# Kernel optimization log

Hardware: AMD Instinct MI355X
Metric: run time of the kernel (lower is better)

The kernel has to match this reference:

```python
import jax, jax.numpy as jnp
import numpy as np

B, IN, H = 4096, 512, 1024
ALPHA, RHO = 0.001, 0.05

def setup_inputs() -> dict:
    key = jax.random.key(0)
    ks = jax.random.split(key, 9)
    inp = jax.random.normal(ks[0], (B, IN), dtype=jnp.float32)
    time = jax.random.uniform(ks[1], (B, 1), dtype=jnp.float32) * 100.0
    hx = jax.random.normal(ks[2], (B, H), dtype=jnp.float32)
    cx = jax.random.normal(ks[3], (B, H), dtype=jnp.float32)
    # params (match torch init scales loosely)
    Wxh_w = jax.random.normal(ks[4], (4 * H, IN), dtype=jnp.float32) / np.sqrt(IN)
    Wxh_b = jnp.zeros((4 * H,), dtype=jnp.float32)
    Whh_w = jax.random.normal(ks[5], (4 * H, H), dtype=jnp.float32) / np.sqrt(H)
    tau = jax.random.normal(ks[6], (H,), dtype=jnp.float32) * 0.5 + 5.0
    s = jax.random.uniform(ks[7], (H,), dtype=jnp.float32) * tau
    alpha = jnp.array([ALPHA], dtype=jnp.float32)
    rho = jnp.array([RHO], dtype=jnp.float32)
    return {"input": inp, "time": time, "hx": hx, "cx": cx,
            "Wxh_w": Wxh_w, "Wxh_b": Wxh_b, "Whh_w": Whh_w,
            "tau": tau, "s": s, "alpha": alpha, "rho": rho}

def _time_gate(time, s, tau, alpha, rho):
    # phi: [B, H] (time [B,1] broadcast against s/tau [H])
    phi = jnp.fmod(time - s, tau) / tau
    k = jnp.where(phi < rho / 2.0, 2.0 * phi / rho,
        jnp.where(phi < rho, 2.0 - 2.0 * phi / rho, alpha * phi))
    # computed under torch.no_grad() in the original
    return jax.lax.stop_gradient(k)

def reference(input, time, hx, cx, Wxh_w, Wxh_b, Whh_w, tau, s, alpha, rho):
    gates = input @ Wxh_w.T + Wxh_b + hx @ Whh_w.T  # [B, 4H]
    i, f, g, o = jnp.split(gates, 4, axis=1)
    k = _time_gate(time, s, tau, alpha, rho)
    ft = jax.nn.sigmoid(f + 1.0 - k)
    it = jax.nn.sigmoid(i) * k
    gt = jnp.tanh(g) * k
    ot = jax.nn.sigmoid(o) * k
    cy = ft * cx + it * gt
    hy = ot * jnp.tanh(cy)
    return (hy, cy)
```

## Files before the change

kernel.cpp:

```cpp
#include <hip/hip_runtime.h>

#define AS1 __attribute__((address_space(1)))
#define AS3 __attribute__((address_space(3)))

typedef _Float16 half_t;
typedef __attribute__((ext_vector_type(8))) _Float16 f16x8;
typedef __attribute__((ext_vector_type(4))) float f32x4;

static constexpr int Bsz = 4096;
static constexpr int INs = 512;
static constexpr int Hs  = 1024;
static constexpr int BM  = 128;
static constexpr int BH  = 32;
static constexpr int BK  = 64;

static constexpr size_t XN  = (size_t)Bsz * INs;
static constexpr size_t HXN = (size_t)Bsz * Hs;
static constexpr size_t WXN = (size_t)4 * Hs * INs;
static constexpr size_t WHN = (size_t)4 * Hs * Hs;
static constexpr size_t OFF_X  = 0;
static constexpr size_t OFF_HX = XN;
static constexpr size_t OFF_WX = XN + HXN;
static constexpr size_t OFF_WH = XN + HXN + WXN;
static constexpr size_t TOT    = XN + HXN + WXN + WHN;
static constexpr size_t KN     = (size_t)Bsz * Hs;

__device__ __forceinline__ float sigm(float x) {
  return 1.0f / (1.0f + __expf(-x));
}
__device__ __forceinline__ float tanh_fast(float x) {
  const float e = __expf(2.0f * x);
  return 1.0f - 2.0f / (e + 1.0f);
}

__global__ __launch_bounds__(256)
void cvt_kernel(const float* __restrict__ x, const float* __restrict__ hx,
                const float* __restrict__ wx, const float* __restrict__ wh,
                const float* __restrict__ timep, const float* __restrict__ sp,
                const float* __restrict__ taup, const float* __restrict__ alphap,
                const float* __restrict__ rhop,
                half_t* __restrict__ ws, float* __restrict__ kout) {
  const size_t cid = (size_t)blockIdx.x * 256 + threadIdx.x;
  if (cid < TOT / 8) {
    const size_t e = cid * 8;
    const float* src; size_t off;
    if (e < OFF_HX)      { src = x;  off = e - OFF_X; }
    else if (e < OFF_WX) { src = hx; off = e - OFF_HX; }
    else if (e < OFF_WH) { src = wx; off = e - OFF_WX; }
    else                 { src = wh; off = e - OFF_WH; }
    const f32x4 a = *(const f32x4*)(src + off);
    const f32x4 b = *(const f32x4*)(src + off + 4);
    f16x8 o;
    o[0]=(half_t)a[0]; o[1]=(half_t)a[1]; o[2]=(half_t)a[2]; o[3]=(half_t)a[3];
    o[4]=(half_t)b[0]; o[5]=(half_t)b[1]; o[6]=(half_t)b[2]; o[7]=(half_t)b[3];
    *(f16x8*)(ws + e) = o;
  } else {
    const size_t e2 = (cid - TOT / 8) * 8;
    const int b = (int)(e2 >> 10);
    const int h = (int)(e2 & 1023);
    const float tv = timep[b];
    const float alphav = alphap[0];
    const float rhov   = rhop[0];
    const float rh     = 0.5f * rhov;
    const f32x4 s0 = *(const f32x4*)(sp + h),   s1 = *(const f32x4*)(sp + h + 4);
    const f32x4 t0 = *(const f32x4*)(taup + h), t1 = *(const f32x4*)(taup + h + 4);
    f32x4 k0, k1;
    #pragma unroll
    for (int j = 0; j < 8; ++j) {
      const float sv   = j < 4 ? s0[j] : s1[j - 4];
      const float tauv = j < 4 ? t0[j] : t1[j - 4];
      const float phi = fmodf(tv - sv, tauv) / tauv;
      float kv;
      if (phi < rh)        kv = (2.0f * phi) / rhov;
      else if (phi < rhov) kv = 2.0f - (2.0f * phi) / rhov;
      else                 kv = alphav * phi;
      if (j < 4) k0[j] = kv; else k1[j - 4] = kv;
    }
    *(f32x4*)(kout + e2) = k0;
    *(f32x4*)(kout + e2 + 4) = k1;
  }
}

template <int MODE>
__global__ __launch_bounds__(256, 3)
void plstm_gemm(const void* __restrict__ xin_,
                const float* __restrict__ timep,
                const void* __restrict__ hxp_,
                const float* __restrict__ cxp,
                const void* __restrict__ wxh_,
                const float* __restrict__ biasp,
                const void* __restrict__ whh_,
                const float* __restrict__ taup,
                const float* __restrict__ sp,
                const float* __restrict__ alphap,
                const float* __restrict__ rhop,
                const float* __restrict__ kp,
                float* __restrict__ outp)
{
  __shared__ half_t As[BM * BK];
  __shared__ half_t Bs[BM * BK];

  const int tid  = threadIdx.x;
  const int w    = tid >> 6;
  const int lane = tid & 63;
  const int l15  = lane & 15;
  const int grp  = lane >> 4;
  const int wr   = w >> 1;
  const int wc   = w & 1;

  const int m0 = blockIdx.x * BM;
  const int h0 = blockIdx.y * BH;

  f32x4 acc[4][4] = {};

  const int ldr = tid >> 3;
  const int ldc = tid & 7;

  for (int phase = 0; phase < 2; ++phase) {
    const void* Ap = (phase == 0) ? xin_ : hxp_;
    const void* Wp = (phase == 0) ? wxh_ : whh_;
    const int Ka = (phase == 0) ? INs : Hs;

    for (int k0 = 0; k0 < Ka; k0 += BK) {
      #pragma unroll
      for (int i = 0; i < 4; ++i) {
        const int e    = i * 32 + ldr;
        const int gc8  = ldc ^ (e & 7);
        const int wrow = ((e >> 4) & 3) * Hs + h0 + ((e >> 6) << 4) + (e & 15);
        if (MODE >= 1) {
          const half_t* ga = (const half_t*)Ap + (size_t)(m0 + e) * Ka + (k0 + gc8 * 8);
          __builtin_amdgcn_global_load_lds((AS1 void*)ga,
                                           (AS3 void*)(As + (e * 8 + ldc) * 8), 16, 0, 0);
          const half_t* gw = (const half_t*)Wp + (size_t)wrow * Ka + (k0 + gc8 * 8);
          __builtin_amdgcn_global_load_lds((AS1 void*)gw,
                                           (AS3 void*)(Bs + (e * 8 + ldc) * 8), 16, 0, 0);
        } else {
          const float* ga = (const float*)Ap + (size_t)(m0 + e) * Ka + (k0 + gc8 * 8);
          const f32x4 a0 = *(const f32x4*)ga, a1 = *(const f32x4*)(ga + 4);
          f16x8 pa;
          pa[0]=(half_t)a0[0]; pa[1]=(half_t)a0[1]; pa[2]=(half_t)a0[2]; pa[3]=(half_t)a0[3];
          pa[4]=(half_t)a1[0]; pa[5]=(half_t)a1[1]; pa[6]=(half_t)a1[2]; pa[7]=(half_t)a1[3];
          *(f16x8*)(As + (e * 8 + ldc) * 8) = pa;
          const float* gw = (const float*)Wp + (size_t)wrow * Ka + (k0 + gc8 * 8);
          const f32x4 b0 = *(const f32x4*)gw, b1 = *(const f32x4*)(gw + 4);
          f16x8 pb;
          pb[0]=(half_t)b0[0]; pb[1]=(half_t)b0[1]; pb[2]=(half_t)b0[2]; pb[3]=(half_t)b0[3];
          pb[4]=(half_t)b1[0]; pb[5]=(half_t)b1[1]; pb[6]=(half_t)b1[2]; pb[7]=(half_t)b1[3];
          *(f16x8*)(Bs + (e * 8 + ldc) * 8) = pb;
        }
      }
      __syncthreads();

      #pragma unroll
      for (int kk = 0; kk < 2; ++kk) {
        const int c8x = (kk * 4 + grp);
        f16x8 af[4], bfr[4];
        #pragma unroll
        for (int mt = 0; mt < 4; ++mt) {
          const int e = wr * 64 + mt * 16 + l15;
          af[mt] = *(const f16x8*)(As + (e * 8 + (c8x ^ (l15 & 7))) * 8);
        }
        #pragma unroll
        for (int nt = 0; nt < 4; ++nt) {
          const int e = wc * 64 + nt * 16 + l15;
          bfr[nt] = *(const f16x8*)(Bs + (e * 8 + (c8x ^ (l15 & 7))) * 8);
        }
        #pragma unroll
        for (int mt = 0; mt < 4; ++mt)
          #pragma unroll
          for (int nt = 0; nt < 4; ++nt)
            acc[mt][nt] = __builtin_amdgcn_mfma_f32_16x16x32_f16(
                af[mt], bfr[nt], acc[mt][nt], 0, 0, 0);
      }
      __syncthreads();
    }
  }

  const int h = h0 + wc * 16 + l15;
  const float bi  = biasp[h];
  const float bfv = biasp[Hs + h];
  const float bg  = biasp[2 * Hs + h];
  const float bo  = biasp[3 * Hs + h];

  float sv = 0.f, tauv = 1.f, alphav = 0.f, rhov = 1.f, rh = 0.f;
  if (MODE < 2) {
    sv = sp[h]; tauv = taup[h];
    alphav = alphap[0]; rhov = rhop[0]; rh = 0.5f * rhov;
  }

  #pragma unroll
  for (int mt = 0; mt < 4; ++mt) {
    #pragma unroll
    for (int r = 0; r < 4; ++r) {
      const int brow = m0 + wr * 64 + mt * 16 + grp * 4 + r;
      float kv;
      if (MODE == 2) {
        kv = kp[(size_t)brow * Hs + h];
      } else {
        const float tv = timep[brow];
        const float phi = fmodf(tv - sv, tauv) / tauv;
        if (phi < rh)        kv = (2.0f * phi) / rhov;
        else if (phi < rhov) kv = 2.0f - (2.0f * phi) / rhov;
        else                 kv = alphav * phi;
      }
      const float iv = acc[mt][0][r] + bi;
      const float fv = acc[mt][1][r] + bfv;
      const float gv = acc[mt][2][r] + bg;
      const float ov = acc[mt][3][r] + bo;

      const float cxv = cxp[(size_t)brow * Hs + h];
      const float ft = sigm(fv + 1.0f - kv);
      const float it = sigm(iv) * kv;
      const float gt = tanh_fast(gv) * kv;
      const float ot = sigm(ov) * kv;
      const float cy = ft * cxv + it * gt;
      const float hy = ot * tanh_fast(cy);

      outp[(size_t)brow * Hs + h] = hy;
      outp[(size_t)Bsz * Hs + (size_t)brow * Hs + h] = cy;
    }
  }
}

extern "C" void kernel_launch(void* const* d_in, const int* in_sizes, int n_in,
                              void* d_out, int out_size, void* d_ws, size_t ws_size,
                              hipStream_t stream) {
  (void)in_sizes; (void)n_in; (void)out_size;
  const float* xin   = (const float*)d_in[0];
  const float* timep = (const float*)d_in[1];
  const float* hxp   = (const float*)d_in[2];
  const float* cxp   = (const float*)d_in[3];
  const float* wxh   = (const float*)d_in[4];
  const float* biasp = (const float*)d_in[5];
  const float* whh   = (const float*)d_in[6];
  const float* taup  = (const float*)d_in[7];
  const float* sp    = (const float*)d_in[8];
  const float* alphap= (const float*)d_in[9];
  const float* rhop  = (const float*)d_in[10];
  float* outp = (float*)d_out;

  dim3 grid(Bsz / BM, Hs / BH);
  const bool wsF16 = ws_size >= TOT * sizeof(half_t);
  const bool wsK   = ws_size >= TOT * sizeof(half_t) + KN * sizeof(float);

  if (wsK) {
    half_t* ws = (half_t*)d_ws;
    float* kout = (float*)(ws + TOT);
    const int nchunk = (int)(TOT / 8 + KN / 8);
    cvt_kernel<<<nchunk / 256, 256, 0, stream>>>(xin, hxp, wxh, whh,
                                                 timep, sp, taup, alphap, rhop,
                                                 ws, kout);
    plstm_gemm<2><<<grid, 256, 0, stream>>>(
        ws + OFF_X, timep, ws + OFF_HX, cxp, ws + OFF_WX, biasp, ws + OFF_WH,
        taup, sp, alphap, rhop, kout, outp);
  } else if (wsF16) {
    half_t* ws = (half_t*)d_ws;
    cvt_kernel<<<(int)(TOT / 8 / 256), 256, 0, stream>>>(xin, hxp, wxh, whh,
                                                 timep, sp, taup, alphap, rhop,
                                                 ws, nullptr);
    plstm_gemm<1><<<grid, 256, 0, stream>>>(
        ws + OFF_X, timep, ws + OFF_HX, cxp, ws + OFF_WX, biasp, ws + OFF_WH,
        taup, sp, alphap, rhop, nullptr, outp);
  } else {
    plstm_gemm<0><<<grid, 256, 0, stream>>>(
        xin, timep, hxp, cxp, wxh, biasp, whh,
        taup, sp, alphap, rhop, nullptr, outp);
  }
}
```

Before: 206.0 us.

## Double-buffer LDS tiles in the fp16 GEMM path with flattened K loop

The fp16 workspace GEMM now keeps two LDS buffers for A and B and issues the asynchronous global-to-LDS loads for the next K tile before computing on the current one. The two phases (input and hidden) are merged into one flattened K loop, so there is one barrier per tile instead of two. This aims to hide global load latency behind the MFMA work. In exchange LDS use doubles and the occupancy hint drops from 3 to 2 blocks per CU. The intermediate fp16-only mode is removed and the fp32 fallback is split out into its own kernel.

Measured after the change: 206.5 us. No clear change (+0.2%).

```diff
diff --git a/kernel.cpp b/kernel.cpp
--- a/kernel.cpp
+++ b/kernel.cpp
@@ -13,6 +13,7 @@
 static constexpr int BM  = 128;
 static constexpr int BH  = 32;
 static constexpr int BK  = 64;
+static constexpr int NIT = INs / BK + Hs / BK;
 
 static constexpr size_t XN  = (size_t)Bsz * INs;
 static constexpr size_t HXN = (size_t)Bsz * Hs;
@@ -81,24 +82,18 @@
   }
 }
 
-template <int MODE>
-__global__ __launch_bounds__(256, 3)
-void plstm_gemm(const void* __restrict__ xin_,
-                const float* __restrict__ timep,
-                const void* __restrict__ hxp_,
-                const float* __restrict__ cxp,
-                const void* __restrict__ wxh_,
-                const float* __restrict__ biasp,
-                const void* __restrict__ whh_,
-                const float* __restrict__ taup,
-                const float* __restrict__ sp,
-                const float* __restrict__ alphap,
-                const float* __restrict__ rhop,
-                const float* __restrict__ kp,
-                float* __restrict__ outp)
+__global__ __launch_bounds__(256, 2)
+void plstm_gemm_db(const half_t* __restrict__ xin,
+                   const half_t* __restrict__ hxp,
+                   const float* __restrict__ cxp,
+                   const half_t* __restrict__ wxh,
+                   const float* __restrict__ biasp,
+                   const half_t* __restrict__ whh,
+                   const float* __restrict__ kp,
+                   float* __restrict__ outp)
 {
-  __shared__ half_t As[BM * BK];
-  __shared__ half_t Bs[BM * BK];
+  __shared__ half_t As[2][BM * BK];
+  __shared__ half_t Bs[2][BM * BK];
 
   const int tid  = threadIdx.x;
   const int w    = tid >> 6;
@@ -116,64 +111,55 @@
   const int ldr = tid >> 3;
   const int ldc = tid & 7;
 
-  for (int phase = 0; phase < 2; ++phase) {
-    const void* Ap = (phase == 0) ? xin_ : hxp_;
-    const void* Wp = (phase == 0) ? wxh_ : whh_;
-    const int Ka = (phase == 0) ? INs : Hs;
-
-    for (int k0 = 0; k0 < Ka; k0 += BK) {
-      #pragma unroll
-      for (int i = 0; i < 4; ++i) {
-        const int e    = i * 32 + ldr;
-        const int gc8  = ldc ^ (e & 7);
-        const int wrow = ((e >> 4) & 3) * Hs + h0 + ((e >> 6) << 4) + (e & 15);
-        if (MODE >= 1) {
-          const half_t* ga = (const half_t*)Ap + (size_t)(m0 + e) * Ka + (k0 + gc8 * 8);
-          __builtin_amdgcn_global_load_lds((AS1 void*)ga,
-                                           (AS3 void*)(As + (e * 8 + ldc) * 8), 16, 0, 0);
-          const half_t* gw = (const half_t*)Wp + (size_t)wrow * Ka + (k0 + gc8 * 8);
-          __builtin_amdgcn_global_load_lds((AS1 void*)gw,
-                                           (AS3 void*)(Bs + (e * 8 + ldc) * 8), 16, 0, 0);
-        } else {
-          const float* ga = (const float*)Ap + (size_t)(m0 + e) * Ka + (k0 + gc8 * 8);
-          const f32x4 a0 = *(const f32x4*)ga, a1 = *(const f32x4*)(ga + 4);
-          f16x8 pa;
-          pa[0]=(half_t)a0[0]; pa[1]=(half_t)a0[1]; pa[2]=(half_t)a0[2]; pa[3]=(half_t)a0[3];
-          pa[4]=(half_t)a1[0]; pa[5]=(half_t)a1[1]; pa[6]=(half_t)a1[2]; pa[7]=(half_t)a1[3];
-          *(f16x8*)(As + (e * 8 + ldc) * 8) = pa;
-          const float* gw = (const float*)Wp + (size_t)wrow * Ka + (k0 + gc8 * 8);
-          const f32x4 b0 = *(const f32x4*)gw, b1 = *(const f32x4*)(gw + 4);
-          f16x8 pb;
-          pb[0]=(half_t)b0[0]; pb[1]=(half_t)b0[1]; pb[2]=(half_t)b0[2]; pb[3]=(half_t)b0[3];
-          pb[4]=(half_t)b1[0]; pb[5]=(half_t)b1[1]; pb[6]=(half_t)b1[2]; pb[7]=(half_t)b1[3];
-          *(f16x8*)(Bs + (e * 8 + ldc) * 8) = pb;
-        }
+  auto stage = [&](int it, int buf) {
+    const bool p1 = it >= INs / BK;
+    const half_t* Ap = p1 ? hxp : xin;
+    const half_t* Wp = p1 ? whh : wxh;
+    const int Ka = p1 ? Hs : INs;
+    const int k0 = (p1 ? (it - INs / BK) : it) * BK;
+    #pragma unroll
+    for (int i = 0; i < 4; ++i) {
+      const int e    = i * 32 + ldr;
+      const int gc8  = ldc ^ (e & 7);
+      const int wrow = ((e >> 4) & 3) * Hs + h0 + ((e >> 6) << 4) + (e & 15);
+      const half_t* ga = Ap + (size_t)(m0 + e) * Ka + (k0 + gc8 * 8);
+      __builtin_amdgcn_global_load_lds((AS1 void*)ga,
+                                       (AS3 void*)(&As[buf][(e * 8 + ldc) * 8]), 16, 0, 0);
+      const half_t* gw = Wp + (size_t)wrow * Ka + (k0 + gc8 * 8);
+      __builtin_amdgcn_global_load_lds((AS1 void*)gw,
+                                       (AS3 void*)(&Bs[buf][(e * 8 + ldc) * 8]), 16, 0, 0);
+    }
+  };
+
+  stage(0, 0);
+  __syncthreads();
+
+  for (int it = 0; it < NIT; ++it) {
+    if (it + 1 < NIT) stage(it + 1, (it + 1) & 1);
+    const half_t* as = As[it & 1];
+    const half_t* bs = Bs[it & 1];
+    #pragma unroll
+    for (int kk = 0; kk < 2; ++kk) {
+      const int c8x = kk * 4 + grp;
+      f16x8 af[4], bfr[4];
+      #pragma unroll
+      for (int mt = 0; mt < 4; ++mt) {
+        const int e = wr * 64 + mt * 16 + l15;
+        af[mt] = *(const f16x8*)(as + (e * 8 + (c8x ^ (l15 & 7))) * 8);
       }
-      __syncthreads();
-
-      #pragma unroll
-      for (int kk = 0; kk < 2; ++kk) {
-        const int c8x = (kk * 4 + grp);
-        f16x8 af[4], bfr[4];
+      #pragma unroll
+      for (int nt = 0; nt < 4; ++nt) {
+        const int e = wc * 64 + nt * 16 + l15;
+        bfr[nt] = *(const f16x8*)(bs + (e * 8 + (c8x ^ (l15 & 7))) * 8);
+      }
+      #pragma unroll
+      for (int mt = 0; mt < 4; ++mt)
         #pragma unroll
-        for (int mt = 0; mt < 4; ++mt) {
-          const int e = wr * 64 + mt * 16 + l15;
-          af[mt] = *(const f16x8*)(As + (e * 8 + (c8x ^ (l15 & 7))) * 8);
-        }
-        #pragma unroll
-        for (int nt = 0; nt < 4; ++nt) {
-          const int e = wc * 64 + nt * 16 + l15;
-          bfr[nt] = *(const f16x8*)(Bs + (e * 8 + (c8x ^ (l15 & 7))) * 8);
-        }
-        #pragma unroll
-        for (int mt = 0; mt < 4; ++mt)
-          #pragma unroll
-          for (int nt = 0; nt < 4; ++nt)
-            acc[mt][nt] = __builtin_amdgcn_mfma_f32_16x16x32_f16(
-                af[mt], bfr[nt], acc[mt][nt], 0, 0, 0);
-      }
-      __syncthreads();
-    }
+        for (int nt = 0; nt < 4; ++nt)
+          acc[mt][nt] = __builtin_amdgcn_mfma_f32_16x16x32_f16(
+              af[mt], bfr[nt], acc[mt][nt], 0, 0, 0);
+    }
+    __syncthreads();
   }
 
   const int h = h0 + wc * 16 + l15;
@@ -182,27 +168,12 @@
   const float bg  = biasp[2 * Hs + h];
   const float bo  = biasp[3 * Hs + h];
 
-  float sv = 0.f, tauv = 1.f, alphav = 0.f, rhov = 1.f, rh = 0.f;
-  if (MODE < 2) {
-    sv = sp[h]; tauv = taup[h];
-    alphav = alphap[0]; rhov = rhop[0]; rh = 0.5f * rhov;
-  }
-
   #pragma unroll
   for (int mt = 0; mt < 4; ++mt) {
     #pragma unroll
     for (int r = 0; r < 4; ++r) {
       const int brow = m0 + wr * 64 + mt * 16 + grp * 4 + r;
-      float kv;
-      if (MODE == 2) {
-        kv = kp[(size_t)brow * Hs + h];
-      } else {
-        const float tv = timep[brow];
-        const float phi = fmodf(tv - sv, tauv) / tauv;
-        if (phi < rh)        kv = (2.0f * phi) / rhov;
-        else if (phi < rhov) kv = 2.0f - (2.0f * phi) / rhov;
-        else                 kv = alphav * phi;
-      }
+      const float kv = kp[(size_t)brow * Hs + h];
       const float iv = acc[mt][0][r] + bi;
       const float fv = acc[mt][1][r] + bfv;
       const float gv = acc[mt][2][r] + bg;
@@ -210,12 +181,123 @@
 
       const float cxv = cxp[(size_t)brow * Hs + h];
       const float ft = sigm(fv + 1.0f - kv);
-      const float it = sigm(iv) * kv;
+      const float it2 = sigm(iv) * kv;
       const float gt = tanh_fast(gv) * kv;
       const float ot = sigm(ov) * kv;
-      const float cy = ft * cxv + it * gt;
+      const float cy = ft * cxv + it2 * gt;
       const float hy = ot * tanh_fast(cy);
 
+      outp[(size_t)brow * Hs + h] = hy;
+      outp[(size_t)Bsz * Hs + (size_t)brow * Hs + h] = cy;
+    }
+  }
+}
+
+__global__ __launch_bounds__(256, 3)
+void plstm_gemm_f32(const float* __restrict__ xin, const float* __restrict__ timep,
+                    const float* __restrict__ hxp, const float* __restrict__ cxp,
+                    const float* __restrict__ wxh, const float* __restrict__ biasp,
+                    const float* __restrict__ whh, const float* __restrict__ taup,
+                    const float* __restrict__ sp, const float* __restrict__ alphap,
+                    const float* __restrict__ rhop, float* __restrict__ outp)
+{
+  __shared__ half_t As[BM * BK];
+  __shared__ half_t Bs[BM * BK];
+
+  const int tid  = threadIdx.x;
+  const int w    = tid >> 6;
+  const int lane = tid & 63;
+  const int l15  = lane & 15;
+  const int grp  = lane >> 4;
+  const int wr   = w >> 1;
+  const int wc   = w & 1;
+
+  const int m0 = blockIdx.x * BM;
+  const int h0 = blockIdx.y * BH;
+
+  f32x4 acc[4][4] = {};
+  const int ldr = tid >> 3;
+  const int ldc = tid & 7;
+
+  for (int it = 0; it < NIT; ++it) {
+    const bool p1 = it >= INs / BK;
+    const float* Ap = p1 ? hxp : xin;
+    const float* Wp = p1 ? whh : wxh;
+    const int Ka = p1 ? Hs : INs;
+    const int k0 = (p1 ? (it - INs / BK) : it) * BK;
+    #pragma unroll
+    for (int i = 0; i < 4; ++i) {
+      const int e    = i * 32 + ldr;
+      const int gc8  = ldc ^ (e & 7);
+      const int wrow = ((e >> 4) & 3) * Hs + h0 + ((e >> 6) << 4) + (e & 15);
+      const float* ga = Ap + (size_t)(m0 + e) * Ka + (k0 + gc8 * 8);
+      const f32x4 a0 = *(const f32x4*)ga, a1 = *(const f32x4*)(ga + 4);
+      f16x8 pa;
+      pa[0]=(half_t)a0[0]; pa[1]=(half_t)a0[1]; pa[2]=(half_t)a0[2]; pa[3]=(half_t)a0[3];
+      pa[4]=(half_t)a1[0]; pa[5]=(half_t)a1[1]; pa[6]=(half_t)a1[2]; pa[7]=(half_t)a1[3];
+      *(f16x8*)(As + (e * 8 + ldc) * 8) = pa;
+      const float* gw = Wp + (size_t)wrow * Ka + (k0 + gc8 * 8);
+      const f32x4 b0 = *(const f32x4*)gw, b1 = *(const f32x4*)(gw + 4);
+      f16x8 pb;
+      pb[0]=(half_t)b0[0]; pb[1]=(half_t)b0[1]; pb[2]=(half_t)b0[2]; pb[3]=(half_t)b0[3];
+      pb[4]=(half_t)b1[0]; pb[5]=(half_t)b1[1]; pb[6]=(half_t)b1[2]; pb[7]=(half_t)b1[3];
+      *(f16x8*)(Bs + (e * 8 + ldc) * 8) = pb;
+    }
+    __syncthreads();
+    #pragma unroll
+    for (int kk = 0; kk < 2; ++kk) {
+      const int c8x = kk * 4 + grp;
+      f16x8 af[4], bfr[4];
+      #pragma unroll
+      for (int mt = 0; mt < 4; ++mt) {
+        const int e = wr * 64 + mt * 16 + l15;
+        af[mt] = *(const f16x8*)(As + (e * 8 + (c8x ^ (l15 & 7))) * 8);
+      }
+      #pragma unroll
+      for (int nt = 0; nt < 4; ++nt) {
+        const int e = wc * 64 + nt * 16 + l15;
+        bfr[nt] = *(const f16x8*)(Bs + (e * 8 + (c8x ^ (l15 & 7))) * 8);
+      }
+      #pragma unroll
+      for (int mt = 0; mt < 4; ++mt)
+        #pragma unroll
+        for (int nt = 0; nt < 4; ++nt)
+          acc[mt][nt] = __builtin_amdgcn_mfma_f32_16x16x32_f16(
+              af[mt], bfr[nt], acc[mt][nt], 0, 0, 0);
+    }
+    __syncthreads();
+  }
+
+  const int h = h0 + wc * 16 + l15;
+  const float bi  = biasp[h];
+  const float bfv = biasp[Hs + h];
+  const float bg  = biasp[2 * Hs + h];
+  const float bo  = biasp[3 * Hs + h];
+  const float sv = sp[h], tauv = taup[h];
+  const float alphav = alphap[0], rhov = rhop[0], rh = 0.5f * rhov;
+
+  #pragma unroll
+  for (int mt = 0; mt < 4; ++mt) {
+    #pragma unroll
+    for (int r = 0; r < 4; ++r) {
+      const int brow = m0 + wr * 64 + mt * 16 + grp * 4 + r;
+      const float tv = timep[brow];
+      const float phi = fmodf(tv - sv, tauv) / tauv;
+      float kv;
+      if (phi < rh)        kv = (2.0f * phi) / rhov;
+      else if (phi < rhov) kv = 2.0f - (2.0f * phi) / rhov;
+      else                 kv = alphav * phi;
+      const float iv = acc[mt][0][r] + bi;
+      const float fv = acc[mt][1][r] + bfv;
+      const float gv = acc[mt][2][r] + bg;
+      const float ov = acc[mt][3][r] + bo;
+      const float cxv = cxp[(size_t)brow * Hs + h];
+      const float ft = sigm(fv + 1.0f - kv);
+      const float it2 = sigm(iv) * kv;
+      const float gt = tanh_fast(gv) * kv;
+      const float ot = sigm(ov) * kv;
+      const float cy = ft * cxv + it2 * gt;
+      const float hy = ot * tanh_fast(cy);
       outp[(size_t)brow * Hs + h] = hy;
       outp[(size_t)Bsz * Hs + (size_t)brow * Hs + h] = cy;
     }
@@ -240,8 +322,7 @@
   float* outp = (float*)d_out;
 
   dim3 grid(Bsz / BM, Hs / BH);
-  const bool wsF16 = ws_size >= TOT * sizeof(half_t);
-  const bool wsK   = ws_size >= TOT * sizeof(half_t) + KN * sizeof(float);
+  const bool wsK = ws_size >= TOT * sizeof(half_t) + KN * sizeof(float);
 
   if (wsK) {
     half_t* ws = (half_t*)d_ws;
@@ -250,20 +331,12 @@
     cvt_kernel<<<nchunk / 256, 256, 0, stream>>>(xin, hxp, wxh, whh,
                                                  timep, sp, taup, alphap, rhop,
                                                  ws, kout);
-    plstm_gemm<2><<<grid, 256, 0, stream>>>(
-        ws + OFF_X, timep, ws + OFF_HX, cxp, ws + OFF_WX, biasp, ws + OFF_WH,
-        taup, sp, alphap, rhop, kout, outp);
-  } else if (wsF16) {
-    half_t* ws = (half_t*)d_ws;
-    cvt_kernel<<<(int)(TOT / 8 / 256), 256, 0, stream>>>(xin, hxp, wxh, whh,
-                                                 timep, sp, taup, alphap, rhop,
-                                                 ws, nullptr);
-    plstm_gemm<1><<<grid, 256, 0, stream>>>(
-        ws + OFF_X, timep, ws + OFF_HX, cxp, ws + OFF_WX, biasp, ws + OFF_WH,
-        taup, sp, alphap, rhop, nullptr, outp);
+    plstm_gemm_db<<<grid, 256, 0, stream>>>(
+        ws + OFF_X, ws + OFF_HX, cxp, ws + OFF_WX, biasp, ws + OFF_WH,
+        kout, outp);
   } else {
-    plstm_gemm<0><<<grid, 256, 0, stream>>>(
+    plstm_gemm_f32<<<grid, 256, 0, stream>>>(
         xin, timep, hxp, cxp, wxh, biasp, whh,
-        taup, sp, alphap, rhop, nullptr, outp);
-  }
-}
+        taup, sp, alphap, rhop, outp);
+  }
+}
```

## Fuse fp32-to-fp16 conversion into GEMM loads and drop pre-conversion kernel

Applied to the files above, without the earlier changes.

Removes the separate conversion kernel that wrote fp16 copies of inputs and weights plus a precomputed time-gate tensor to workspace. The single fused kernel now loads fp32 directly, converts to fp16 in registers before storing to LDS, and computes the time gate inline. It also flattens the two-phase K loop into one loop and raises the occupancy hint to 4 blocks per SM. This avoids an extra pass over the weights and activations, but the GEMM now reads fp32 (twice the bytes) for every tile, repeatedly across blocks, and loses the async global-to-LDS loads.

Measured after the change: 215.5 us. 4.6% more time.

```diff
diff --git a/kernel.cpp b/kernel.cpp
--- a/kernel.cpp
+++ b/kernel.cpp
@@ -1,7 +1,4 @@
 #include <hip/hip_runtime.h>
-
-#define AS1 __attribute__((address_space(1)))
-#define AS3 __attribute__((address_space(3)))
 
 typedef _Float16 half_t;
 typedef __attribute__((ext_vector_type(8))) _Float16 f16x8;
@@ -13,17 +10,7 @@
 static constexpr int BM  = 128;
 static constexpr int BH  = 32;
 static constexpr int BK  = 64;
-
-static constexpr size_t XN  = (size_t)Bsz * INs;
-static constexpr size_t HXN = (size_t)Bsz * Hs;
-static constexpr size_t WXN = (size_t)4 * Hs * INs;
-static constexpr size_t WHN = (size_t)4 * Hs * Hs;
-static constexpr size_t OFF_X  = 0;
-static constexpr size_t OFF_HX = XN;
-static constexpr size_t OFF_WX = XN + HXN;
-static constexpr size_t OFF_WH = XN + HXN + WXN;
-static constexpr size_t TOT    = XN + HXN + WXN + WHN;
-static constexpr size_t KN     = (size_t)Bsz * Hs;
+static constexpr int NIT = INs / BK + Hs / BK;
 
 __device__ __forceinline__ float sigm(float x) {
   return 1.0f / (1.0f + __expf(-x));
@@ -33,69 +20,19 @@
   return 1.0f - 2.0f / (e + 1.0f);
 }
 
-__global__ __launch_bounds__(256)
-void cvt_kernel(const float* __restrict__ x, const float* __restrict__ hx,
-                const float* __restrict__ wx, const float* __restrict__ wh,
-                const float* __restrict__ timep, const float* __restrict__ sp,
-                const float* __restrict__ taup, const float* __restrict__ alphap,
-                const float* __restrict__ rhop,
-                half_t* __restrict__ ws, float* __restrict__ kout) {
-  const size_t cid = (size_t)blockIdx.x * 256 + threadIdx.x;
-  if (cid < TOT / 8) {
-    const size_t e = cid * 8;
-    const float* src; size_t off;
-    if (e < OFF_HX)      { src = x;  off = e - OFF_X; }
-    else if (e < OFF_WX) { src = hx; off = e - OFF_HX; }
-    else if (e < OFF_WH) { src = wx; off = e - OFF_WX; }
-    else                 { src = wh; off = e - OFF_WH; }
-    const f32x4 a = *(const f32x4*)(src + off);
-    const f32x4 b = *(const f32x4*)(src + off + 4);
-    f16x8 o;
-    o[0]=(half_t)a[0]; o[1]=(half_t)a[1]; o[2]=(half_t)a[2]; o[3]=(half_t)a[3];
-    o[4]=(half_t)b[0]; o[5]=(half_t)b[1]; o[6]=(half_t)b[2]; o[7]=(half_t)b[3];
-    *(f16x8*)(ws + e) = o;
-  } else {
-    const size_t e2 = (cid - TOT / 8) * 8;
-    const int b = (int)(e2 >> 10);
-    const int h = (int)(e2 & 1023);
-    const float tv = timep[b];
-    const float alphav = alphap[0];
-    const float rhov   = rhop[0];
-    const float rh     = 0.5f * rhov;
-    const f32x4 s0 = *(const f32x4*)(sp + h),   s1 = *(const f32x4*)(sp + h + 4);
-    const f32x4 t0 = *(const f32x4*)(taup + h), t1 = *(const f32x4*)(taup + h + 4);
-    f32x4 k0, k1;
-    #pragma unroll
-    for (int j = 0; j < 8; ++j) {
-      const float sv   = j < 4 ? s0[j] : s1[j - 4];
-      const float tauv = j < 4 ? t0[j] : t1[j - 4];
-      const float phi = fmodf(tv - sv, tauv) / tauv;
-      float kv;
-      if (phi < rh)        kv = (2.0f * phi) / rhov;
-      else if (phi < rhov) kv = 2.0f - (2.0f * phi) / rhov;
-      else                 kv = alphav * phi;
-      if (j < 4) k0[j] = kv; else k1[j - 4] = kv;
-    }
-    *(f32x4*)(kout + e2) = k0;
-    *(f32x4*)(kout + e2 + 4) = k1;
-  }
-}
-
-template <int MODE>
-__global__ __launch_bounds__(256, 3)
-void plstm_gemm(const void* __restrict__ xin_,
-                const float* __restrict__ timep,
-                const void* __restrict__ hxp_,
-                const float* __restrict__ cxp,
-                const void* __restrict__ wxh_,
-                const float* __restrict__ biasp,
-                const void* __restrict__ whh_,
-                const float* __restrict__ taup,
-                const float* __restrict__ sp,
-                const float* __restrict__ alphap,
-                const float* __restrict__ rhop,
-                const float* __restrict__ kp,
-                float* __restrict__ outp)
+__global__ __launch_bounds__(256, 4)
+void plstm_fused(const float* __restrict__ xin,
+                 const float* __restrict__ timep,
+                 const float* __restrict__ hxp,
+                 const float* __restrict__ cxp,
+                 const float* __restrict__ wxh,
+                 const float* __restrict__ biasp,
+                 const float* __restrict__ whh,
+                 const float* __restrict__ taup,
+                 const float* __restrict__ sp,
+                 const float* __restrict__ alphap,
+                 const float* __restrict__ rhop,
+                 float* __restrict__ outp)
 {
   __shared__ half_t As[BM * BK];
   __shared__ half_t Bs[BM * BK];
@@ -116,64 +53,54 @@
   const int ldr = tid >> 3;
   const int ldc = tid & 7;
 
-  for (int phase = 0; phase < 2; ++phase) {
-    const void* Ap = (phase == 0) ? xin_ : hxp_;
-    const void* Wp = (phase == 0) ? wxh_ : whh_;
-    const int Ka = (phase == 0) ? INs : Hs;
+  for (int it = 0; it < NIT; ++it) {
+    const bool p1 = it >= INs / BK;
+    const float* Ap = p1 ? hxp : xin;
+    const float* Wp = p1 ? whh : wxh;
+    const int Ka = p1 ? Hs : INs;
+    const int k0 = (p1 ? (it - INs / BK) : it) * BK;
+    #pragma unroll
+    for (int i = 0; i < 4; ++i) {
+      const int e    = i * 32 + ldr;
+      const int gc8  = ldc ^ (e & 7);
+      const int wrow = ((e >> 4) & 3) * Hs + h0 + ((e >> 6) << 4) + (e & 15);
+      const float* ga = Ap + (size_t)(m0 + e) * Ka + (k0 + gc8 * 8);
+      const f32x4 a0 = *(const f32x4*)ga, a1 = *(const f32x4*)(ga + 4);
+      f16x8 pa;
+      pa[0]=(half_t)a0[0]; pa[1]=(half_t)a0[1]; pa[2]=(half_t)a0[2]; pa[3]=(half_t)a0[3];
+      pa[4]=(half_t)a1[0]; pa[5]=(half_t)a1[1]; pa[6]=(half_t)a1[2]; pa[7]=(half_t)a1[3];
+      *(f16x8*)(As + (e * 8 + ldc) * 8) = pa;
+      const float* gw = Wp + (size_t)wrow * Ka + (k0 + gc8 * 8);
+      const f32x4 b0 = *(const f32x4*)gw, b1 = *(const f32x4*)(gw + 4);
+      f16x8 pb;
+      pb[0]=(half_t)b0[0]; pb[1]=(half_t)b0[1]; pb[2]=(half_t)b0[2]; pb[3]=(half_t)b0[3];
+      pb[4]=(half_t)b1[0]; pb[5]=(half_t)b1[1]; pb[6]=(half_t)b1[2]; pb[7]=(half_t)b1[3];
+      *(f16x8*)(Bs + (e * 8 + ldc) * 8) = pb;
+    }
+    __syncthreads();
 
-    for (int k0 = 0; k0 < Ka; k0 += BK) {
+    #pragma unroll
+    for (int kk = 0; kk < 2; ++kk) {
+      const int c8x = kk * 4 + grp;
+      f16x8 af[4], bfr[4];
       #pragma unroll
-      for (int i = 0; i < 4; ++i) {
-        const int e    = i * 32 + ldr;
-        const int gc8  = ldc ^ (e & 7);
-        const int wrow = ((e >> 4) & 3) * Hs + h0 + ((e >> 6) << 4) + (e & 15);
-        if (MODE >= 1) {
-          const half_t* ga = (const half_t*)Ap + (size_t)(m0 + e) * Ka + (k0 + gc8 * 8);
-          __builtin_amdgcn_global_load_lds((AS1 void*)ga,
-                                           (AS3 void*)(As + (e * 8 + ldc) * 8), 16, 0, 0);
-          const half_t* gw = (const half_t*)Wp + (size_t)wrow * Ka + (k0 + gc8 * 8);
-          __builtin_amdgcn_global_load_lds((AS1 void*)gw,
-                                           (AS3 void*)(Bs + (e * 8 + ldc) * 8), 16, 0, 0);
-        } else {
-          const float* ga = (const float*)Ap + (size_t)(m0 + e) * Ka + (k0 + gc8 * 8);
-          const f32x4 a0 = *(const f32x4*)ga, a1 = *(const f32x4*)(ga + 4);
-          f16x8 pa;
-          pa[0]=(half_t)a0[0]; pa[1]=(half_t)a0[1]; pa[2]=(half_t)a0[2]; pa[3]=(half_t)a0[3];
-          pa[4]=(half_t)a1[0]; pa[5]=(half_t)a1[1]; pa[6]=(half_t)a1[2]; pa[7]=(half_t)a1[3];
-          *(f16x8*)(As + (e * 8 + ldc) * 8) = pa;
-          const float* gw = (const float*)Wp + (size_t)wrow * Ka + (k0 + gc8 * 8);
-          const f32x4 b0 = *(const f32x4*)gw, b1 = *(const f32x4*)(gw + 4);
-          f16x8 pb;
-          pb[0]=(half_t)b0[0]; pb[1]=(half_t)b0[1]; pb[2]=(half_t)b0[2]; pb[3]=(half_t)b0[3];
-          pb[4]=(half_t)b1[0]; pb[5]=(half_t)b1[1]; pb[6]=(half_t)b1[2]; pb[7]=(half_t)b1[3];
-          *(f16x8*)(Bs + (e * 8 + ldc) * 8) = pb;
-        }
+      for (int mt = 0; mt < 4; ++mt) {
+        const int e = wr * 64 + mt * 16 + l15;
+        af[mt] = *(const f16x8*)(As + (e * 8 + (c8x ^ (l15 & 7))) * 8);
       }
-      __syncthreads();
-
       #pragma unroll
-      for (int kk = 0; kk < 2; ++kk) {
-        const int c8x = (kk * 4 + grp);
-        f16x8 af[4], bfr[4];
+      for (int nt = 0; nt < 4; ++nt) {
+        const int e = wc * 64 + nt * 16 + l15;
+        bfr[nt] = *(const f16x8*)(Bs + (e * 8 + (c8x ^ (l15 & 7))) * 8);
+      }
+      #pragma unroll
+      for (int mt = 0; mt < 4; ++mt)
         #pragma unroll
-        for (int mt = 0; mt < 4; ++mt) {
-          const int e = wr * 64 + mt * 16 + l15;
-          af[mt] = *(const f16x8*)(As + (e * 8 + (c8x ^ (l15 & 7))) * 8);
-        }
-        #pragma unroll
-        for (int nt = 0; nt < 4; ++nt) {
-          const int e = wc * 64 + nt * 16 + l15;
-          bfr[nt] = *(const f16x8*)(Bs + (e * 8 + (c8x ^ (l15 & 7))) * 8);
-        }
-        #pragma unroll
-        for (int mt = 0; mt < 4; ++mt)
-          #pragma unroll
-          for (int nt = 0; nt < 4; ++nt)
-            acc[mt][nt] = __builtin_amdgcn_mfma_f32_16x16x32_f16(
-                af[mt], bfr[nt], acc[mt][nt], 0, 0, 0);
-      }
-      __syncthreads();
+        for (int nt = 0; nt < 4; ++nt)
+          acc[mt][nt] = __builtin_amdgcn_mfma_f32_16x16x32_f16(
+              af[mt], bfr[nt], acc[mt][nt], 0, 0, 0);
     }
+    __syncthreads();
   }
 
   const int h = h0 + wc * 16 + l15;
@@ -181,39 +108,31 @@
   const float bfv = biasp[Hs + h];
   const float bg  = biasp[2 * Hs + h];
   const float bo  = biasp[3 * Hs + h];
-
-  float sv = 0.f, tauv = 1.f, alphav = 0.f, rhov = 1.f, rh = 0.f;
-  if (MODE < 2) {
-    sv = sp[h]; tauv = taup[h];
-    alphav = alphap[0]; rhov = rhop[0]; rh = 0.5f * rhov;
-  }
+  const float sv = sp[h], tauv = taup[h];
+  const float alphav = alphap[0], rhov = rhop[0], rh = 0.5f * rhov;
 
   #pragma unroll
   for (int mt = 0; mt < 4; ++mt) {
     #pragma unroll
     for (int r = 0; r < 4; ++r) {
       const int brow = m0 + wr * 64 + mt * 16 + grp * 4 + r;
+      const float tv = timep[brow];
+      const float phi = fmodf(tv - sv, tauv) / tauv;
       float kv;
-      if (MODE == 2) {
-        kv = kp[(size_t)brow * Hs + h];
-      } else {
-        const float tv = timep[brow];
-        const float phi = fmodf(tv - sv, tauv) / tauv;
-        if (phi < rh)        kv = (2.0f * phi) / rhov;
-        else if (phi < rhov) kv = 2.0f - (2.0f * phi) / rhov;
-        else                 kv = alphav * phi;
-      }
+      if (phi < rh)        kv = (2.0f * phi) / rhov;
+      else if (phi < rhov) kv = 2.0f - (2.0f * phi) / rhov;
+      else                 kv = alphav * phi;
+
       const float iv = acc[mt][0][r] + bi;
       const float fv = acc[mt][1][r] + bfv;
       const float gv = acc[mt][2][r] + bg;
       const float ov = acc[mt][3][r] + bo;
-
       const float cxv = cxp[(size_t)brow * Hs + h];
       const float ft = sigm(fv + 1.0f - kv);
-      const float it = sigm(iv) * kv;
+      const float it2 = sigm(iv) * kv;
       const float gt = tanh_fast(gv) * kv;
       const float ot = sigm(ov) * kv;
-      const float cy = ft * cxv + it * gt;
+      const float cy = ft * cxv + it2 * gt;
       const float hy = ot * tanh_fast(cy);
 
       outp[(size_t)brow * Hs + h] = hy;
@@ -225,45 +144,12 @@
 extern "C" void kernel_launch(void* const* d_in, const int* in_sizes, int n_in,
                               void* d_out, int out_size, void* d_ws, size_t ws_size,
                               hipStream_t stream) {
-  (void)in_sizes; (void)n_in; (void)out_size;
-  const float* xin   = (const float*)d_in[0];
-  const float* timep = (const float*)d_in[1];
-  const float* hxp   = (const float*)d_in[2];
-  const float* cxp   = (const float*)d_in[3];
-  const float* wxh   = (const float*)d_in[4];
-  const float* biasp = (const float*)d_in[5];
-  const float* whh   = (const float*)d_in[6];
-  const float* taup  = (const float*)d_in[7];
-  const float* sp    = (const float*)d_in[8];
-  const float* alphap= (const float*)d_in[9];
-  const float* rhop  = (const float*)d_in[10];
-  float* outp = (float*)d_out;
-
+  (void)in_sizes; (void)n_in; (void)out_size; (void)d_ws; (void)ws_size;
   dim3 grid(Bsz / BM, Hs / BH);
-  const bool wsF16 = ws_size >= TOT * sizeof(half_t);
-  const bool wsK   = ws_size >= TOT * sizeof(half_t) + KN * sizeof(float);
-
-  if (wsK) {
-    half_t* ws = (half_t*)d_ws;
-    float* kout = (float*)(ws + TOT);
-    const int nchunk = (int)(TOT / 8 + KN / 8);
-    cvt_kernel<<<nchunk / 256, 256, 0, stream>>>(xin, hxp, wxh, whh,
-                                                 timep, sp, taup, alphap, rhop,
-                                                 ws, kout);
-    plstm_gemm<2><<<grid, 256, 0, stream>>>(
-        ws + OFF_X, timep, ws + OFF_HX, cxp, ws + OFF_WX, biasp, ws + OFF_WH,
-        taup, sp, alphap, rhop, kout, outp);
-  } else if (wsF16) {
-    half_t* ws = (half_t*)d_ws;
-    cvt_kernel<<<(int)(TOT / 8 / 256), 256, 0, stream>>>(xin, hxp, wxh, whh,
-                                                 timep, sp, taup, alphap, rhop,
-                                                 ws, nullptr);
-    plstm_gemm<1><<<grid, 256, 0, stream>>>(
-        ws + OFF_X, timep, ws + OFF_HX, cxp, ws + OFF_WX, biasp, ws + OFF_WH,
-        taup, sp, alphap, rhop, nullptr, outp);
-  } else {
-    plstm_gemm<0><<<grid, 256, 0, stream>>>(
-        xin, timep, hxp, cxp, wxh, biasp, whh,
-        taup, sp, alphap, rhop, nullptr, outp);
-  }
+  plstm_fused<<<grid, 256, 0, stream>>>(
+      (const float*)d_in[0], (const float*)d_in[1], (const float*)d_in[2],
+      (const float*)d_in[3], (const float*)d_in[4], (const float*)d_in[5],
+      (const float*)d_in[6], (const float*)d_in[7], (const float*)d_in[8],
+      (const float*)d_in[9], (const float*)d_in[10],
+      (float*)d_out);
 }
```
